# Optimization experiments

Measured on AMD Instinct MI355X. Metric: run time of the kernel, lower is better.

The kernel has to match this reference:

```python
import jax, jax.numpy as jnp
import numpy as np

D_MODEL = 1024
D_HID = D_MODEL // 4
N_EXPERTS = 64
TOP_K = 2


def setup_inputs() -> dict:
    key = jax.random.key(0)
    k_x, k_w1, k_b1, k_w2, k_b2 = jax.random.split(key, 5)
    # torch Linear default init: U(-1/sqrt(fan_in), 1/sqrt(fan_in))
    s1 = 1.0 / np.sqrt(D_MODEL)
    s2 = 1.0 / np.sqrt(D_HID)
    return {
        "x": jax.random.normal(k_x, (4, 4096, D_MODEL), dtype=jnp.float32),
        "W1": jax.random.uniform(k_w1, (D_MODEL, D_HID), jnp.float32, -s1, s1),
        "b1": jax.random.uniform(k_b1, (D_HID,), jnp.float32, -s1, s1),
        "W2": jax.random.uniform(k_w2, (D_HID, N_EXPERTS), jnp.float32, -s2, s2),
        "b2": jax.random.uniform(k_b2, (N_EXPERTS,), jnp.float32, -s2, s2),
    }


def reference(x, W1, b1, W2, b2):
    # gate MLP: [B,S,D] -> [B,S,H] -> tanh -> [B,S,E]
    h = jnp.tanh(jnp.einsum("bsd,dh->bsh", x, W1) + b1)
    gate_logits = jnp.einsum("bsh,he->bse", h, W2) + b2
    # top-k selection + softmax over the k selected logits
    top_logits, top_idx = jax.lax.top_k(gate_logits, TOP_K)  # [B,S,K]
    top_gates = jax.nn.softmax(top_logits, axis=-1)          # [B,S,K]
    # scatter back into dense [B,S,E] gate tensor
    onehot = jax.nn.one_hot(top_idx, N_EXPERTS, dtype=top_gates.dtype)  # [B,S,K,E]
    gates = jnp.einsum("bsk,bske->bse", top_gates, onehot)
    return gates, gate_logits
```

## Files before the change

kernel.cpp:

```cpp
#include <hip/hip_runtime.h>
#include <math.h>


#define DM 1024
#define DH 256
#define NE 64

#define W1P_OFF 0
#define W1P_STRIDE 524288
#define W2P_OFF 1572864
#define W2P_STRIDE 32768

#define HSTR 276
#define AROW 80
#define APLANE 2560
#define ABUF 7680

typedef __attribute__((ext_vector_type(8))) short bf16x8;
typedef __attribute__((ext_vector_type(4))) float f32x4;

__device__ __forceinline__ unsigned fbits(float f) { return __float_as_uint(f); }
__device__ __forceinline__ float topf(unsigned u) { return __uint_as_float(u & 0xFFFF0000u); }

__device__ __forceinline__ void split3(float v, unsigned& h, unsigned& m, unsigned& l) {
    h = fbits(v);
    float r1 = v - topf(h);
    m = fbits(r1);
    float r2 = r1 - topf(m);
    l = fbits(r2);
}
__device__ __forceinline__ unsigned packpair(unsigned a, unsigned b) {
    return (a >> 16) | (b & 0xFFFF0000u);
}
__device__ __forceinline__ bf16x8 as_bf(uint4 u) {
    union { uint4 a; bf16x8 b; } c; c.a = u; return c.b;
}

__device__ __forceinline__ void split_pack8(float4 f0, float4 f1,
                                            bf16x8& H, bf16x8& M, bf16x8& L) {
    float v[8] = {f0.x, f0.y, f0.z, f0.w, f1.x, f1.y, f1.z, f1.w};
    unsigned hb[8], mb[8], lb[8];
#pragma unroll
    for (int j = 0; j < 8; j++) split3(v[j], hb[j], mb[j], lb[j]);
    uint4 uh = {packpair(hb[0], hb[1]), packpair(hb[2], hb[3]),
                packpair(hb[4], hb[5]), packpair(hb[6], hb[7])};
    uint4 um = {packpair(mb[0], mb[1]), packpair(mb[2], mb[3]),
                packpair(mb[4], mb[5]), packpair(mb[6], mb[7])};
    uint4 ul = {packpair(lb[0], lb[1]), packpair(lb[2], lb[3]),
                packpair(lb[4], lb[5]), packpair(lb[6], lb[7])};
    H = as_bf(uh); M = as_bf(um); L = as_bf(ul);
}


__global__ __launch_bounds__(256)
void prep_planes(const float* __restrict__ W1, const float* __restrict__ W2,
                 char* __restrict__ ws) {
    __shared__ float tile[512];
    unsigned* w1p = (unsigned*)(ws + W1P_OFF);
    unsigned* w2p = (unsigned*)(ws + W2P_OFF);
    const int b = blockIdx.x, t = threadIdx.x;
    const int q = t & 3, L = (t >> 2) & 63;
    const int n_loc = L & 15;
    const int k_loc = ((L >> 4) & 3) * 8 + 2 * q;
    if (b < 512) {
        const int kc = b >> 4, nt = b & 15;
#pragma unroll
        for (int i = 0; i < 2; i++) {
            const int idx = t + i * 256;
            tile[idx] = W1[(size_t)(kc * 32 + (idx >> 4)) * DH + nt * 16 + (idx & 15)];
        }
        __syncthreads();
        const float v0 = tile[k_loc * 16 + n_loc];
        const float v1 = tile[(k_loc + 1) * 16 + n_loc];
        unsigned h0, m0, l0, h1, m1, l1;
        split3(v0, h0, m0, l0);
        split3(v1, h1, m1, l1);
        const int gt = b * 256 + t;
        w1p[0 * 131072 + gt] = packpair(h0, h1);
        w1p[1 * 131072 + gt] = packpair(m0, m1);
        w1p[2 * 131072 + gt] = packpair(l0, l1);
    } else {
        const int b2 = b - 512;
        const int kc = b2 >> 2, nt = b2 & 3;
#pragma unroll
        for (int i = 0; i < 2; i++) {
            const int idx = t + i * 256;
            tile[idx] = W2[(kc * 32 + (idx >> 4)) * NE + nt * 16 + (idx & 15)];
        }
        __syncthreads();
        const float v0 = tile[k_loc * 16 + n_loc];
        const float v1 = tile[(k_loc + 1) * 16 + n_loc];
        unsigned h0, m0, l0, h1, m1, l1;
        split3(v0, h0, m0, l0);
        split3(v1, h1, m1, l1);
        const int g2 = b2 * 256 + t;
        w2p[0 * 8192 + g2] = packpair(h0, h1);
        w2p[1 * 8192 + g2] = packpair(m0, m1);
        w2p[2 * 8192 + g2] = packpair(l0, l1);
    }
}

__global__ __launch_bounds__(512, 4)
void fused_gating(const float* __restrict__ x, const char* __restrict__ w1p,
                  const float* __restrict__ b1, const char* __restrict__ w2p,
                  const float* __restrict__ b2, float* __restrict__ gates,
                  float* __restrict__ logits_out) {
    __shared__ __align__(16) char alds[2 * ABUF];
    __shared__ __align__(16) float hlds[32 * HSTR];

    const int tid  = threadIdx.x;
    const int lane = tid & 63;
    const int wave = tid >> 6;
    const int m15 = lane & 15;
    const int lq  = lane >> 4;
    const int t0 = blockIdx.x * 32;

    const int stok = tid >> 4;
    const int skp  = (tid & 15) * 2;
    const float* xs = x + (size_t)(t0 + stok) * DM + skp;
    const int swoff = stok * AROW + (tid & 15) * 4;

    const char* bbase = w1p + (size_t)(wave * 2) * 1024 + lane * 16;

    f32x4 acc[2][2];
#pragma unroll
    for (int ms = 0; ms < 2; ms++)
#pragma unroll
        for (int nt = 0; nt < 2; nt++) acc[ms][nt] = (f32x4){0.f, 0.f, 0.f, 0.f};

    {
        float2 v = *(const float2*)(xs);
        unsigned h0, m0, l0, h1, m1, l1;
        split3(v.x, h0, m0, l0);
        split3(v.y, h1, m1, l1);
        *(unsigned*)(alds + 0 * APLANE + swoff) = packpair(h0, h1);
        *(unsigned*)(alds + 1 * APLANE + swoff) = packpair(m0, m1);
        *(unsigned*)(alds + 2 * APLANE + swoff) = packpair(l0, l1);
    }
    float2 xc = *(const float2*)(xs + 32);
    uint4 bc[3][2];
#pragma unroll
    for (int p = 0; p < 3; p++)
#pragma unroll
        for (int nt = 0; nt < 2; nt++)
            bc[p][nt] = *(const uint4*)(bbase + p * W1P_STRIDE + nt * 1024);
    __syncthreads();

#pragma unroll 2
    for (int kc = 0; kc < 32; kc++) {
        const int k2 = (kc + 2) & 31;
        const int k1 = (kc + 1) & 31;
        float2 xn = *(const float2*)(xs + k2 * 32);
        uint4 bn[3][2];
#pragma unroll
        for (int p = 0; p < 3; p++)
#pragma unroll
            for (int nt = 0; nt < 2; nt++)
                bn[p][nt] = *(const uint4*)(bbase + p * W1P_STRIDE + k1 * 16384 + nt * 1024);

        const char* ab = alds + (kc & 1) * ABUF + m15 * AROW + lq * 16;
        const bf16x8 a0h = *(const bf16x8*)(ab + 0 * APLANE);
        const bf16x8 a0m = *(const bf16x8*)(ab + 1 * APLANE);
        const bf16x8 a0l = *(const bf16x8*)(ab + 2 * APLANE);
        const bf16x8 a1h = *(const bf16x8*)(ab + 0 * APLANE + 16 * AROW);
        const bf16x8 a1m = *(const bf16x8*)(ab + 1 * APLANE + 16 * AROW);
        const bf16x8 a1l = *(const bf16x8*)(ab + 2 * APLANE + 16 * AROW);

#pragma unroll
        for (int nt = 0; nt < 2; nt++) {
            const bf16x8 bh = as_bf(bc[0][nt]);
            const bf16x8 bm = as_bf(bc[1][nt]);
            const bf16x8 bl = as_bf(bc[2][nt]);
            f32x4 a0 = acc[0][nt];
            a0 = __builtin_amdgcn_mfma_f32_16x16x32_bf16(a0h, bh, a0, 0, 0, 0);
            a0 = __builtin_amdgcn_mfma_f32_16x16x32_bf16(a0h, bm, a0, 0, 0, 0);
            a0 = __builtin_amdgcn_mfma_f32_16x16x32_bf16(a0m, bh, a0, 0, 0, 0);
            a0 = __builtin_amdgcn_mfma_f32_16x16x32_bf16(a0h, bl, a0, 0, 0, 0);
            a0 = __builtin_amdgcn_mfma_f32_16x16x32_bf16(a0l, bh, a0, 0, 0, 0);
            a0 = __builtin_amdgcn_mfma_f32_16x16x32_bf16(a0m, bm, a0, 0, 0, 0);
            acc[0][nt] = a0;
            f32x4 a1 = acc[1][nt];
            a1 = __builtin_amdgcn_mfma_f32_16x16x32_bf16(a1h, bh, a1, 0, 0, 0);
            a1 = __builtin_amdgcn_mfma_f32_16x16x32_bf16(a1h, bm, a1, 0, 0, 0);
            a1 = __builtin_amdgcn_mfma_f32_16x16x32_bf16(a1m, bh, a1, 0, 0, 0);
            a1 = __builtin_amdgcn_mfma_f32_16x16x32_bf16(a1h, bl, a1, 0, 0, 0);
            a1 = __builtin_amdgcn_mfma_f32_16x16x32_bf16(a1l, bh, a1, 0, 0, 0);
            a1 = __builtin_amdgcn_mfma_f32_16x16x32_bf16(a1m, bm, a1, 0, 0, 0);
            acc[1][nt] = a1;
        }

        {
            char* wb = alds + ((kc + 1) & 1) * ABUF + swoff;
            unsigned h0, m0, l0, h1, m1, l1;
            split3(xc.x, h0, m0, l0);
            split3(xc.y, h1, m1, l1);
            *(unsigned*)(wb + 0 * APLANE) = packpair(h0, h1);
            *(unsigned*)(wb + 1 * APLANE) = packpair(m0, m1);
            *(unsigned*)(wb + 2 * APLANE) = packpair(l0, l1);
        }
        xc = xn;
#pragma unroll
        for (int p = 0; p < 3; p++)
#pragma unroll
            for (int nt = 0; nt < 2; nt++) bc[p][nt] = bn[p][nt];
        __syncthreads();
    }

#pragma unroll
    for (int nt = 0; nt < 2; nt++) {
        const int hid = wave * 32 + nt * 16 + m15;
        const float bias = b1[hid];
#pragma unroll
        for (int ms = 0; ms < 2; ms++) {
            const int tb = ms * 16 + lq * 4;
#pragma unroll
            for (int r = 0; r < 4; r++)
                hlds[(tb + r) * HSTR + hid] = tanhf(acc[ms][nt][r] + bias);
        }
    }
    __syncthreads();

    if (wave < 2) {
        const float* hb = hlds + (wave * 16 + m15) * HSTR + lq * 8;
        const char* bt = w2p + lane * 16;

        f32x4 gacc[4];
#pragma unroll
        for (int nt = 0; nt < 4; nt++) gacc[nt] = (f32x4){0.f, 0.f, 0.f, 0.f};

#pragma unroll
        for (int kc = 0; kc < 8; kc++) {
            float4 f0 = *(const float4*)(hb + kc * 32);
            float4 f1 = *(const float4*)(hb + kc * 32 + 4);
            bf16x8 afh, afm, afl;
            split_pack8(f0, f1, afh, afm, afl);
#pragma unroll
            for (int nt = 0; nt < 4; nt++) {
                const char* tb = bt + (kc * 4 + nt) * 1024;
                bf16x8 bh = *(const bf16x8*)(tb + 0 * W2P_STRIDE);
                bf16x8 bm = *(const bf16x8*)(tb + 1 * W2P_STRIDE);
                bf16x8 bl = *(const bf16x8*)(tb + 2 * W2P_STRIDE);
                f32x4 a = gacc[nt];
                a = __builtin_amdgcn_mfma_f32_16x16x32_bf16(afh, bh, a, 0, 0, 0);
                a = __builtin_amdgcn_mfma_f32_16x16x32_bf16(afh, bm, a, 0, 0, 0);
                a = __builtin_amdgcn_mfma_f32_16x16x32_bf16(afm, bh, a, 0, 0, 0);
                a = __builtin_amdgcn_mfma_f32_16x16x32_bf16(afh, bl, a, 0, 0, 0);
                a = __builtin_amdgcn_mfma_f32_16x16x32_bf16(afl, bh, a, 0, 0, 0);
                a = __builtin_amdgcn_mfma_f32_16x16x32_bf16(afm, bm, a, 0, 0, 0);
                gacc[nt] = a;
            }
        }

        float b2v[4];
#pragma unroll
        for (int nt = 0; nt < 4; nt++) b2v[nt] = b2[nt * 16 + m15];

#pragma unroll
        for (int r = 0; r < 4; r++) {
            float v[4]; int e[4];
#pragma unroll
            for (int nt = 0; nt < 4; nt++) { v[nt] = gacc[nt][r] + b2v[nt]; e[nt] = nt * 16 + m15; }

            float a1 = v[0], a2 = v[1]; int j1 = e[0], j2 = e[1];
            if (v[1] > v[0]) { a1 = v[1]; j1 = e[1]; a2 = v[0]; j2 = e[0]; }
#pragma unroll
            for (int t = 2; t < 4; t++) {
                if (v[t] > a1) { a2 = a1; j2 = j1; a1 = v[t]; j1 = e[t]; }
                else if (v[t] > a2) { a2 = v[t]; j2 = e[t]; }
            }
#pragma unroll
            for (int off = 1; off < 16; off <<= 1) {
                float ob1 = __shfl_xor(a1, off, 64); int oj1 = __shfl_xor(j1, off, 64);
                float ob2 = __shfl_xor(a2, off, 64); int oj2 = __shfl_xor(j2, off, 64);
                bool bw = (ob1 > a1) || (ob1 == a1 && oj1 < j1);
                float w1v = bw ? ob1 : a1; int w1i = bw ? oj1 : j1;
                float lv = bw ? a1 : ob1;  int li  = bw ? j1 : oj1;
                float rv = bw ? ob2 : a2;  int ri  = bw ? oj2 : j2;
                bool cw = (lv > rv) || (lv == rv && li < ri);
                a1 = w1v; j1 = w1i;
                a2 = cw ? lv : rv; j2 = cw ? li : ri;
            }
            float ex = __expf(a2 - a1);
            float inv = 1.f / (1.f + ex);
            float g1 = inv, g2 = ex * inv;

            const size_t row = (size_t)(t0 + wave * 16 + lq * 4 + r) * NE;
#pragma unroll
            for (int nt = 0; nt < 4; nt++) {
                float gv = (e[nt] == j1) ? g1 : ((e[nt] == j2) ? g2 : 0.f);
                gates[row + e[nt]] = gv;
                logits_out[row + e[nt]] = v[nt];
            }
        }
    }
}

extern "C" void kernel_launch(void* const* d_in, const int* in_sizes, int n_in,
                              void* d_out, int out_size, void* d_ws, size_t ws_size,
                              hipStream_t stream) {
    const float* x  = (const float*)d_in[0];
    const float* W1 = (const float*)d_in[1];
    const float* b1 = (const float*)d_in[2];
    const float* W2 = (const float*)d_in[3];
    const float* b2 = (const float*)d_in[4];

    const int T = in_sizes[0] / DM;
    char* ws = (char*)d_ws;
    float* gates  = (float*)d_out;
    float* logits = (float*)d_out + (size_t)T * NE;

    prep_planes<<<512 + 32, 256, 0, stream>>>(W1, W2, ws);
    fused_gating<<<T / 32, 512, 0, stream>>>(x, ws + W1P_OFF, b1, ws + W2P_OFF, b2,
                                             gates, logits);
}
```

Measured before the change: 150.6 us.

## Double K-chunk per iteration with float4 x staging and halved barriers

The GEMM main loop now handles 64 K-elements per iteration instead of 32, staging x as float4 per thread into a wider LDS row. This halves the number of __syncthreads barriers and makes global x loads wider. W1 fragments for both halves are loaded directly at the top of each iteration instead of being register-prefetched one step ahead, and x is prefetched three steps ahead. The trade-off is more LDS per block, higher register pressure, and less latency hiding for the B loads.

```diff
diff --git a/kernel.cpp b/kernel.cpp
--- a/kernel.cpp
+++ b/kernel.cpp
@@ -12,9 +12,9 @@
 #define W2P_STRIDE 32768
 
 #define HSTR 276
-#define AROW 80
-#define APLANE 2560
-#define ABUF 7680
+#define AROW 144
+#define APLANE 4608
+#define ABUF 13824
 
 typedef __attribute__((ext_vector_type(8))) short bf16x8;
 typedef __attribute__((ext_vector_type(4))) float f32x4;
@@ -34,6 +34,20 @@
 }
 __device__ __forceinline__ bf16x8 as_bf(uint4 u) {
     union { uint4 a; bf16x8 b; } c; c.a = u; return c.b;
+}
+
+__device__ __forceinline__ void stage4(float4 f, char* wb) {
+    unsigned h[4], m[4], l[4];
+    split3(f.x, h[0], m[0], l[0]);
+    split3(f.y, h[1], m[1], l[1]);
+    split3(f.z, h[2], m[2], l[2]);
+    split3(f.w, h[3], m[3], l[3]);
+    uint2 dh = {packpair(h[0], h[1]), packpair(h[2], h[3])};
+    uint2 dm = {packpair(m[0], m[1]), packpair(m[2], m[3])};
+    uint2 dl = {packpair(l[0], l[1]), packpair(l[2], l[3])};
+    *(uint2*)(wb + 0 * APLANE) = dh;
+    *(uint2*)(wb + 1 * APLANE) = dm;
+    *(uint2*)(wb + 2 * APLANE) = dl;
 }
 
 __device__ __forceinline__ void split_pack8(float4 f0, float4 f1,
@@ -116,9 +130,9 @@
     const int t0 = blockIdx.x * 32;
 
     const int stok = tid >> 4;
-    const int skp  = (tid & 15) * 2;
-    const float* xs = x + (size_t)(t0 + stok) * DM + skp;
-    const int swoff = stok * AROW + (tid & 15) * 4;
+    const int seg  = tid & 15;
+    const float* xs = x + (size_t)(t0 + stok) * DM + seg * 4;
+    const int swoff = stok * AROW + seg * 8;
 
     const char* bbase = w1p + (size_t)(wave * 2) * 1024 + lane * 16;
 
@@ -128,81 +142,89 @@
 #pragma unroll
         for (int nt = 0; nt < 2; nt++) acc[ms][nt] = (f32x4){0.f, 0.f, 0.f, 0.f};
 
-    {
-        float2 v = *(const float2*)(xs);
-        unsigned h0, m0, l0, h1, m1, l1;
-        split3(v.x, h0, m0, l0);
-        split3(v.y, h1, m1, l1);
-        *(unsigned*)(alds + 0 * APLANE + swoff) = packpair(h0, h1);
-        *(unsigned*)(alds + 1 * APLANE + swoff) = packpair(m0, m1);
-        *(unsigned*)(alds + 2 * APLANE + swoff) = packpair(l0, l1);
-    }
-    float2 xc = *(const float2*)(xs + 32);
-    uint4 bc[3][2];
-#pragma unroll
-    for (int p = 0; p < 3; p++)
-#pragma unroll
-        for (int nt = 0; nt < 2; nt++)
-            bc[p][nt] = *(const uint4*)(bbase + p * W1P_STRIDE + nt * 1024);
+    stage4(*(const float4*)(xs), alds + swoff);
+    float4 xc  = *(const float4*)(xs + 64);
+    float4 xc2 = *(const float4*)(xs + 128);
     __syncthreads();
 
 #pragma unroll 2
-    for (int kc = 0; kc < 32; kc++) {
-        const int k2 = (kc + 2) & 31;
-        const int k1 = (kc + 1) & 31;
-        float2 xn = *(const float2*)(xs + k2 * 32);
-        uint4 bn[3][2];
+    for (int t = 0; t < 16; t++) {
+        const int kcA = 2 * t, kcB = 2 * t + 1;
+        uint4 b0[3][2], b1f[3][2];
 #pragma unroll
         for (int p = 0; p < 3; p++)
 #pragma unroll
-            for (int nt = 0; nt < 2; nt++)
-                bn[p][nt] = *(const uint4*)(bbase + p * W1P_STRIDE + k1 * 16384 + nt * 1024);
-
-        const char* ab = alds + (kc & 1) * ABUF + m15 * AROW + lq * 16;
-        const bf16x8 a0h = *(const bf16x8*)(ab + 0 * APLANE);
-        const bf16x8 a0m = *(const bf16x8*)(ab + 1 * APLANE);
-        const bf16x8 a0l = *(const bf16x8*)(ab + 2 * APLANE);
-        const bf16x8 a1h = *(const bf16x8*)(ab + 0 * APLANE + 16 * AROW);
-        const bf16x8 a1m = *(const bf16x8*)(ab + 1 * APLANE + 16 * AROW);
-        const bf16x8 a1l = *(const bf16x8*)(ab + 2 * APLANE + 16 * AROW);
-
-#pragma unroll
-        for (int nt = 0; nt < 2; nt++) {
-            const bf16x8 bh = as_bf(bc[0][nt]);
-            const bf16x8 bm = as_bf(bc[1][nt]);
-            const bf16x8 bl = as_bf(bc[2][nt]);
-            f32x4 a0 = acc[0][nt];
-            a0 = __builtin_amdgcn_mfma_f32_16x16x32_bf16(a0h, bh, a0, 0, 0, 0);
-            a0 = __builtin_amdgcn_mfma_f32_16x16x32_bf16(a0h, bm, a0, 0, 0, 0);
-            a0 = __builtin_amdgcn_mfma_f32_16x16x32_bf16(a0m, bh, a0, 0, 0, 0);
-            a0 = __builtin_amdgcn_mfma_f32_16x16x32_bf16(a0h, bl, a0, 0, 0, 0);
-            a0 = __builtin_amdgcn_mfma_f32_16x16x32_bf16(a0l, bh, a0, 0, 0, 0);
-            a0 = __builtin_amdgcn_mfma_f32_16x16x32_bf16(a0m, bm, a0, 0, 0, 0);
-            acc[0][nt] = a0;
-            f32x4 a1 = acc[1][nt];
-            a1 = __builtin_amdgcn_mfma_f32_16x16x32_bf16(a1h, bh, a1, 0, 0, 0);
-            a1 = __builtin_amdgcn_mfma_f32_16x16x32_bf16(a1h, bm, a1, 0, 0, 0);
-            a1 = __builtin_amdgcn_mfma_f32_16x16x32_bf16(a1m, bh, a1, 0, 0, 0);
-            a1 = __builtin_amdgcn_mfma_f32_16x16x32_bf16(a1h, bl, a1, 0, 0, 0);
-            a1 = __builtin_amdgcn_mfma_f32_16x16x32_bf16(a1l, bh, a1, 0, 0, 0);
-            a1 = __builtin_amdgcn_mfma_f32_16x16x32_bf16(a1m, bm, a1, 0, 0, 0);
-            acc[1][nt] = a1;
-        }
+            for (int nt = 0; nt < 2; nt++) {
+                b0[p][nt]  = *(const uint4*)(bbase + p * W1P_STRIDE + kcA * 16384 + nt * 1024);
+                b1f[p][nt] = *(const uint4*)(bbase + p * W1P_STRIDE + kcB * 16384 + nt * 1024);
+            }
+        float4 xn = *(const float4*)(xs + ((t + 3) & 15) * 64);
+
+        const char* ab = alds + (t & 1) * ABUF + m15 * AROW + lq * 16;
 
         {
-            char* wb = alds + ((kc + 1) & 1) * ABUF + swoff;
-            unsigned h0, m0, l0, h1, m1, l1;
-            split3(xc.x, h0, m0, l0);
-            split3(xc.y, h1, m1, l1);
-            *(unsigned*)(wb + 0 * APLANE) = packpair(h0, h1);
-            *(unsigned*)(wb + 1 * APLANE) = packpair(m0, m1);
-            *(unsigned*)(wb + 2 * APLANE) = packpair(l0, l1);
-        }
-        xc = xn;
-#pragma unroll
-        for (int p = 0; p < 3; p++)
-#pragma unroll
-            for (int nt = 0; nt < 2; nt++) bc[p][nt] = bn[p][nt];
+            const bf16x8 a0h = *(const bf16x8*)(ab + 0 * APLANE);
+            const bf16x8 a0m = *(const bf16x8*)(ab + 1 * APLANE);
+            const bf16x8 a0l = *(const bf16x8*)(ab + 2 * APLANE);
+            const bf16x8 a1h = *(const bf16x8*)(ab + 0 * APLANE + 16 * AROW);
+            const bf16x8 a1m = *(const bf16x8*)(ab + 1 * APLANE + 16 * AROW);
+            const bf16x8 a1l = *(const bf16x8*)(ab + 2 * APLANE + 16 * AROW);
+#pragma unroll
+            for (int nt = 0; nt < 2; nt++) {
+                const bf16x8 bh = as_bf(b0[0][nt]);
+                const bf16x8 bm = as_bf(b0[1][nt]);
+                const bf16x8 bl = as_bf(b0[2][nt]);
+                f32x4 a0 = acc[0][nt];
+                a0 = __builtin_amdgcn_mfma_f32_16x16x32_bf16(a0h, bh, a0, 0, 0, 0);
+                a0 = __builtin_amdgcn_mfma_f32_16x16x32_bf16(a0h, bm, a0, 0, 0, 0);
+                a0 = __builtin_amdgcn_mfma_f32_16x16x32_bf16(a0m, bh, a0, 0, 0, 0);
+                a0 = __builtin_amdgcn_mfma_f32_16x16x32_bf16(a0h, bl, a0, 0, 0, 0);
+                a0 = __builtin_amdgcn_mfma_f32_16x16x32_bf16(a0l, bh, a0, 0, 0, 0);
+                a0 = __builtin_amdgcn_mfma_f32_16x16x32_bf16(a0m, bm, a0, 0, 0, 0);
+                acc[0][nt] = a0;
+                f32x4 a1 = acc[1][nt];
+                a1 = __builtin_amdgcn_mfma_f32_16x16x32_bf16(a1h, bh, a1, 0, 0, 0);
+                a1 = __builtin_amdgcn_mfma_f32_16x16x32_bf16(a1h, bm, a1, 0, 0, 0);
+                a1 = __builtin_amdgcn_mfma_f32_16x16x32_bf16(a1m, bh, a1, 0, 0, 0);
+                a1 = __builtin_amdgcn_mfma_f32_16x16x32_bf16(a1h, bl, a1, 0, 0, 0);
+                a1 = __builtin_amdgcn_mfma_f32_16x16x32_bf16(a1l, bh, a1, 0, 0, 0);
+                a1 = __builtin_amdgcn_mfma_f32_16x16x32_bf16(a1m, bm, a1, 0, 0, 0);
+                acc[1][nt] = a1;
+            }
+        }
+        {
+            const bf16x8 a0h = *(const bf16x8*)(ab + 0 * APLANE + 64);
+            const bf16x8 a0m = *(const bf16x8*)(ab + 1 * APLANE + 64);
+            const bf16x8 a0l = *(const bf16x8*)(ab + 2 * APLANE + 64);
+            const bf16x8 a1h = *(const bf16x8*)(ab + 0 * APLANE + 16 * AROW + 64);
+            const bf16x8 a1m = *(const bf16x8*)(ab + 1 * APLANE + 16 * AROW + 64);
+            const bf16x8 a1l = *(const bf16x8*)(ab + 2 * APLANE + 16 * AROW + 64);
+#pragma unroll
+            for (int nt = 0; nt < 2; nt++) {
+                const bf16x8 bh = as_bf(b1f[0][nt]);
+                const bf16x8 bm = as_bf(b1f[1][nt]);
+                const bf16x8 bl = as_bf(b1f[2][nt]);
+                f32x4 a0 = acc[0][nt];
+                a0 = __builtin_amdgcn_mfma_f32_16x16x32_bf16(a0h, bh, a0, 0, 0, 0);
+                a0 = __builtin_amdgcn_mfma_f32_16x16x32_bf16(a0h, bm, a0, 0, 0, 0);
+                a0 = __builtin_amdgcn_mfma_f32_16x16x32_bf16(a0m, bh, a0, 0, 0, 0);
+                a0 = __builtin_amdgcn_mfma_f32_16x16x32_bf16(a0h, bl, a0, 0, 0, 0);
+                a0 = __builtin_amdgcn_mfma_f32_16x16x32_bf16(a0l, bh, a0, 0, 0, 0);
+                a0 = __builtin_amdgcn_mfma_f32_16x16x32_bf16(a0m, bm, a0, 0, 0, 0);
+                acc[0][nt] = a0;
+                f32x4 a1 = acc[1][nt];
+                a1 = __builtin_amdgcn_mfma_f32_16x16x32_bf16(a1h, bh, a1, 0, 0, 0);
+                a1 = __builtin_amdgcn_mfma_f32_16x16x32_bf16(a1h, bm, a1, 0, 0, 0);
+                a1 = __builtin_amdgcn_mfma_f32_16x16x32_bf16(a1m, bh, a1, 0, 0, 0);
+                a1 = __builtin_amdgcn_mfma_f32_16x16x32_bf16(a1h, bl, a1, 0, 0, 0);
+                a1 = __builtin_amdgcn_mfma_f32_16x16x32_bf16(a1l, bh, a1, 0, 0, 0);
+                a1 = __builtin_amdgcn_mfma_f32_16x16x32_bf16(a1m, bm, a1, 0, 0, 0);
+                acc[1][nt] = a1;
+            }
+        }
+
+        stage4(xc, alds + ((t + 1) & 1) * ABUF + swoff);
+        xc = xc2; xc2 = xn;
         __syncthreads();
     }
 
```

Result: no change. 149.3 us (-0.8%).

## Double token tile to 64 per block to halve W1 plane reloads

Applied to the files above, without the earlier changes.

Each block now processes 64 tokens instead of 32, so every W1 bf16-plane fragment loaded from global memory feeds four M-subtiles instead of two, halving total W1 traffic across the grid. Staging uses float4 loads with a two-step-ahead x prefetch. The W1 register double-buffer is dropped in favour of in-iteration loads. The A and H shared buffers are aliased into one allocation and launch bounds are relaxed to 2 blocks per CU. In exchange there are twice as many accumulator registers, fewer blocks (256 for 16K tokens, about one wave of blocks on the GPU), and less latency hiding for the W1 loads.

```diff
diff --git a/kernel.cpp b/kernel.cpp
--- a/kernel.cpp
+++ b/kernel.cpp
@@ -13,8 +13,9 @@
 
 #define HSTR 276
 #define AROW 80
-#define APLANE 2560
-#define ABUF 7680
+#define APLANE 5120
+#define ABUF 15360
+#define SMEM_BYTES 70656
 
 typedef __attribute__((ext_vector_type(8))) short bf16x8;
 typedef __attribute__((ext_vector_type(4))) float f32x4;
@@ -34,6 +35,20 @@
 }
 __device__ __forceinline__ bf16x8 as_bf(uint4 u) {
     union { uint4 a; bf16x8 b; } c; c.a = u; return c.b;
+}
+
+__device__ __forceinline__ void stage4(float4 f, char* wb) {
+    unsigned h[4], m[4], l[4];
+    split3(f.x, h[0], m[0], l[0]);
+    split3(f.y, h[1], m[1], l[1]);
+    split3(f.z, h[2], m[2], l[2]);
+    split3(f.w, h[3], m[3], l[3]);
+    uint2 dh = {packpair(h[0], h[1]), packpair(h[2], h[3])};
+    uint2 dm = {packpair(m[0], m[1]), packpair(m[2], m[3])};
+    uint2 dl = {packpair(l[0], l[1]), packpair(l[2], l[3])};
+    *(uint2*)(wb + 0 * APLANE) = dh;
+    *(uint2*)(wb + 1 * APLANE) = dm;
+    *(uint2*)(wb + 2 * APLANE) = dl;
 }
 
 __device__ __forceinline__ void split_pack8(float4 f0, float4 f1,
@@ -100,109 +115,82 @@
     }
 }
 
-__global__ __launch_bounds__(512, 4)
+__global__ __launch_bounds__(512, 2)
 void fused_gating(const float* __restrict__ x, const char* __restrict__ w1p,
                   const float* __restrict__ b1, const char* __restrict__ w2p,
                   const float* __restrict__ b2, float* __restrict__ gates,
                   float* __restrict__ logits_out) {
-    __shared__ __align__(16) char alds[2 * ABUF];
-    __shared__ __align__(16) float hlds[32 * HSTR];
+    __shared__ __align__(16) char smem[SMEM_BYTES];
+    char* alds = smem;
+    float* hlds = (float*)smem;
 
     const int tid  = threadIdx.x;
     const int lane = tid & 63;
     const int wave = tid >> 6;
     const int m15 = lane & 15;
     const int lq  = lane >> 4;
-    const int t0 = blockIdx.x * 32;
-
-    const int stok = tid >> 4;
-    const int skp  = (tid & 15) * 2;
-    const float* xs = x + (size_t)(t0 + stok) * DM + skp;
-    const int swoff = stok * AROW + (tid & 15) * 4;
+    const int t0 = blockIdx.x * 64;
+
+    const int stok = tid >> 3;
+    const int seg  = tid & 7;
+    const float* xs = x + (size_t)(t0 + stok) * DM + seg * 4;
+    const int swoff = stok * AROW + seg * 8;
 
     const char* bbase = w1p + (size_t)(wave * 2) * 1024 + lane * 16;
 
-    f32x4 acc[2][2];
-#pragma unroll
-    for (int ms = 0; ms < 2; ms++)
+    f32x4 acc[4][2];
+#pragma unroll
+    for (int ms = 0; ms < 4; ms++)
 #pragma unroll
         for (int nt = 0; nt < 2; nt++) acc[ms][nt] = (f32x4){0.f, 0.f, 0.f, 0.f};
 
-    {
-        float2 v = *(const float2*)(xs);
-        unsigned h0, m0, l0, h1, m1, l1;
-        split3(v.x, h0, m0, l0);
-        split3(v.y, h1, m1, l1);
-        *(unsigned*)(alds + 0 * APLANE + swoff) = packpair(h0, h1);
-        *(unsigned*)(alds + 1 * APLANE + swoff) = packpair(m0, m1);
-        *(unsigned*)(alds + 2 * APLANE + swoff) = packpair(l0, l1);
-    }
-    float2 xc = *(const float2*)(xs + 32);
-    uint4 bc[3][2];
-#pragma unroll
-    for (int p = 0; p < 3; p++)
-#pragma unroll
-        for (int nt = 0; nt < 2; nt++)
-            bc[p][nt] = *(const uint4*)(bbase + p * W1P_STRIDE + nt * 1024);
+    stage4(*(const float4*)(xs), alds + swoff);
+    float4 xc  = *(const float4*)(xs + 32);
+    float4 xc2 = *(const float4*)(xs + 64);
     __syncthreads();
 
 #pragma unroll 2
     for (int kc = 0; kc < 32; kc++) {
-        const int k2 = (kc + 2) & 31;
-        const int k1 = (kc + 1) & 31;
-        float2 xn = *(const float2*)(xs + k2 * 32);
-        uint4 bn[3][2];
+        uint4 bc[3][2];
 #pragma unroll
         for (int p = 0; p < 3; p++)
 #pragma unroll
             for (int nt = 0; nt < 2; nt++)
-                bn[p][nt] = *(const uint4*)(bbase + p * W1P_STRIDE + k1 * 16384 + nt * 1024);
+                bc[p][nt] = *(const uint4*)(bbase + p * W1P_STRIDE + kc * 16384 + nt * 1024);
+        float4 xn = *(const float4*)(xs + ((kc + 3) & 31) * 32);
+
+        if (kc < 31)
+            stage4(xc, alds + ((kc + 1) & 1) * ABUF + swoff);
+        xc = xc2; xc2 = xn;
 
         const char* ab = alds + (kc & 1) * ABUF + m15 * AROW + lq * 16;
-        const bf16x8 a0h = *(const bf16x8*)(ab + 0 * APLANE);
-        const bf16x8 a0m = *(const bf16x8*)(ab + 1 * APLANE);
-        const bf16x8 a0l = *(const bf16x8*)(ab + 2 * APLANE);
-        const bf16x8 a1h = *(const bf16x8*)(ab + 0 * APLANE + 16 * AROW);
-        const bf16x8 a1m = *(const bf16x8*)(ab + 1 * APLANE + 16 * AROW);
-        const bf16x8 a1l = *(const bf16x8*)(ab + 2 * APLANE + 16 * AROW);
-
-#pragma unroll
-        for (int nt = 0; nt < 2; nt++) {
-            const bf16x8 bh = as_bf(bc[0][nt]);
-            const bf16x8 bm = as_bf(bc[1][nt]);
-            const bf16x8 bl = as_bf(bc[2][nt]);
-            f32x4 a0 = acc[0][nt];
-            a0 = __builtin_amdgcn_mfma_f32_16x16x32_bf16(a0h, bh, a0, 0, 0, 0);
-            a0 = __builtin_amdgcn_mfma_f32_16x16x32_bf16(a0h, bm, a0, 0, 0, 0);
-            a0 = __builtin_amdgcn_mfma_f32_16x16x32_bf16(a0m, bh, a0, 0, 0, 0);
-            a0 = __builtin_amdgcn_mfma_f32_16x16x32_bf16(a0h, bl, a0, 0, 0, 0);
-            a0 = __builtin_amdgcn_mfma_f32_16x16x32_bf16(a0l, bh, a0, 0, 0, 0);
-            a0 = __builtin_amdgcn_mfma_f32_16x16x32_bf16(a0m, bm, a0, 0, 0, 0);
-            acc[0][nt] = a0;
-            f32x4 a1 = acc[1][nt];
-            a1 = __builtin_amdgcn_mfma_f32_16x16x32_bf16(a1h, bh, a1, 0, 0, 0);
-            a1 = __builtin_amdgcn_mfma_f32_16x16x32_bf16(a1h, bm, a1, 0, 0, 0);
-            a1 = __builtin_amdgcn_mfma_f32_16x16x32_bf16(a1m, bh, a1, 0, 0, 0);
-            a1 = __builtin_amdgcn_mfma_f32_16x16x32_bf16(a1h, bl, a1, 0, 0, 0);
-            a1 = __builtin_amdgcn_mfma_f32_16x16x32_bf16(a1l, bh, a1, 0, 0, 0);
-            a1 = __builtin_amdgcn_mfma_f32_16x16x32_bf16(a1m, bm, a1, 0, 0, 0);
-            acc[1][nt] = a1;
-        }
-
-        {
-            char* wb = alds + ((kc + 1) & 1) * ABUF + swoff;
-            unsigned h0, m0, l0, h1, m1, l1;
-            split3(xc.x, h0, m0, l0);
-            split3(xc.y, h1, m1, l1);
-            *(unsigned*)(wb + 0 * APLANE) = packpair(h0, h1);
-            *(unsigned*)(wb + 1 * APLANE) = packpair(m0, m1);
-            *(unsigned*)(wb + 2 * APLANE) = packpair(l0, l1);
-        }
-        xc = xn;
-#pragma unroll
-        for (int p = 0; p < 3; p++)
-#pragma unroll
-            for (int nt = 0; nt < 2; nt++) bc[p][nt] = bn[p][nt];
+        bf16x8 af[4][3];
+#pragma unroll
+        for (int ms = 0; ms < 4; ms++)
+#pragma unroll
+            for (int p = 0; p < 3; p++)
+                af[ms][p] = *(const bf16x8*)(ab + p * APLANE + ms * (16 * AROW));
+
+#pragma unroll
+        for (int ms = 0; ms < 4; ms++)
+#pragma unroll
+            for (int nt = 0; nt < 2; nt++) {
+                const bf16x8 ah = af[ms][0];
+                const bf16x8 am = af[ms][1];
+                const bf16x8 al = af[ms][2];
+                const bf16x8 bh = as_bf(bc[0][nt]);
+                const bf16x8 bm = as_bf(bc[1][nt]);
+                const bf16x8 bl = as_bf(bc[2][nt]);
+                f32x4 a = acc[ms][nt];
+                a = __builtin_amdgcn_mfma_f32_16x16x32_bf16(ah, bh, a, 0, 0, 0);
+                a = __builtin_amdgcn_mfma_f32_16x16x32_bf16(ah, bm, a, 0, 0, 0);
+                a = __builtin_amdgcn_mfma_f32_16x16x32_bf16(am, bh, a, 0, 0, 0);
+                a = __builtin_amdgcn_mfma_f32_16x16x32_bf16(ah, bl, a, 0, 0, 0);
+                a = __builtin_amdgcn_mfma_f32_16x16x32_bf16(al, bh, a, 0, 0, 0);
+                a = __builtin_amdgcn_mfma_f32_16x16x32_bf16(am, bm, a, 0, 0, 0);
+                acc[ms][nt] = a;
+            }
+
         __syncthreads();
     }
 
@@ -211,7 +199,7 @@
         const int hid = wave * 32 + nt * 16 + m15;
         const float bias = b1[hid];
 #pragma unroll
-        for (int ms = 0; ms < 2; ms++) {
+        for (int ms = 0; ms < 4; ms++) {
             const int tb = ms * 16 + lq * 4;
 #pragma unroll
             for (int r = 0; r < 4; r++)
@@ -220,7 +208,7 @@
     }
     __syncthreads();
 
-    if (wave < 2) {
+    if (wave < 4) {
         const float* hb = hlds + (wave * 16 + m15) * HSTR + lq * 8;
         const char* bt = w2p + lane * 16;
 
@@ -264,9 +252,9 @@
             float a1 = v[0], a2 = v[1]; int j1 = e[0], j2 = e[1];
             if (v[1] > v[0]) { a1 = v[1]; j1 = e[1]; a2 = v[0]; j2 = e[0]; }
 #pragma unroll
-            for (int t = 2; t < 4; t++) {
-                if (v[t] > a1) { a2 = a1; j2 = j1; a1 = v[t]; j1 = e[t]; }
-                else if (v[t] > a2) { a2 = v[t]; j2 = e[t]; }
+            for (int tt = 2; tt < 4; tt++) {
+                if (v[tt] > a1) { a2 = a1; j2 = j1; a1 = v[tt]; j1 = e[tt]; }
+                else if (v[tt] > a2) { a2 = v[tt]; j2 = e[tt]; }
             }
 #pragma unroll
             for (int off = 1; off < 16; off <<= 1) {
@@ -310,6 +298,6 @@
     float* logits = (float*)d_out + (size_t)T * NE;
 
     prep_planes<<<512 + 32, 256, 0, stream>>>(W1, W2, ws);
-    fused_gating<<<T / 32, 512, 0, stream>>>(x, ws + W1P_OFF, b1, ws + W2P_OFF, b2,
+    fused_gating<<<T / 64, 512, 0, stream>>>(x, ws + W1P_OFF, b1, ws + W2P_OFF, b2,
                                              gates, logits);
 }
```

Measured after the change: 145.7 us. 1.03x faster.
